# Optimization experiments

Measured on AMD Instinct MI355X. Metric: run time of the kernel, lower is better.

The kernel has to match this reference:

```python
import jax, jax.numpy as jnp
import numpy as np

NUM_GRAPHS = 64
NODE_SZ = 200
FEAT = 200
HID = 256          # hidden_size; each signed branch outputs HID//2
HALF = HID // 2
N_NODES = NUM_GRAPHS * NODE_SZ
N_EDGES = 409600
NUM_LAYERS = 3


def _lin_init(key, out_f, in_f):
    kw, kb = jax.random.split(key)
    s = 1.0 / np.sqrt(in_f)
    W = jax.random.uniform(kw, (out_f, in_f), minval=-s, maxval=s, dtype=jnp.float32)
    b = jax.random.uniform(kb, (out_f,), minval=-s, maxval=s, dtype=jnp.float32)
    return W, b


def setup_inputs() -> dict:
    key = jax.random.key(0)
    ks = jax.random.split(key, 16)
    x = jax.random.normal(ks[0], (N_NODES, FEAT), dtype=jnp.float32)
    edge_index = jax.random.randint(ks[1], (2, N_EDGES), 0, N_NODES, dtype=jnp.int64)
    edge_weight = jax.random.normal(ks[2], (N_EDGES,), dtype=jnp.float32)
    batch = jnp.repeat(jnp.arange(NUM_GRAPHS, dtype=jnp.int64), NODE_SZ)

    # signed conv layer params: layer0 in=FEAT, layers 1..: in=HID; each lin maps 2*in -> HALF
    Wp0, bp0 = _lin_init(ks[3], HALF, 2 * FEAT)
    Wn0, bn0 = _lin_init(ks[4], HALF, 2 * FEAT)
    Wp1, bp1 = _lin_init(ks[5], HALF, 2 * HID)
    Wn1, bn1 = _lin_init(ks[6], HALF, 2 * HID)
    Wp2, bp2 = _lin_init(ks[7], HALF, 2 * HID)
    Wn2, bn2 = _lin_init(ks[8], HALF, 2 * HID)
    Wr, br = _lin_init(ks[9], HID, NODE_SZ * HID)   # readout_lin
    Wl, bl = _lin_init(ks[10], 1, HID)              # final lin
    return dict(x=x, edge_index=edge_index, edge_weight=edge_weight, batch=batch,
                Wp0=Wp0, bp0=bp0, Wn0=Wn0, bn0=bn0,
                Wp1=Wp1, bp1=bp1, Wn1=Wn1, bn1=bn1,
                Wp2=Wp2, bp2=bp2, Wn2=Wn2, bn2=bn2,
                Wr=Wr, br=br, Wl=Wl, bl=bl)


def _signed_conv(x, src, dst, w, Wp, bp, Wn, bn):
    # edge-weighted signed mean aggregation, split by weight sign
    xs = x[src]                                   # [E, D] gather
    pw = jnp.where(w > 0, w, 0.0)
    nw = jnp.where(w < 0, -w, 0.0)
    agg_p = jax.ops.segment_sum(pw[:, None] * xs, dst, num_segments=N_NODES)
    agg_n = jax.ops.segment_sum(nw[:, None] * xs, dst, num_segments=N_NODES)
    deg_p = jax.ops.segment_sum((w > 0).astype(x.dtype), dst, num_segments=N_NODES)
    deg_n = jax.ops.segment_sum((w < 0).astype(x.dtype), dst, num_segments=N_NODES)
    agg_p = agg_p / jnp.maximum(deg_p, 1.0)[:, None]
    agg_n = agg_n / jnp.maximum(deg_n, 1.0)[:, None]
    hp = jnp.concatenate([agg_p, x], -1) @ Wp.T + bp
    hn = jnp.concatenate([agg_n, x], -1) @ Wn.T + bn
    return jnp.concatenate([hp, hn], -1)          # [N, HID]


def reference(x, edge_index, edge_weight, batch,
              Wp0, bp0, Wn0, bn0, Wp1, bp1, Wn1, bn1, Wp2, bp2, Wn2, bn2,
              Wr, br, Wl, bl):
    src, dst = edge_index[0], edge_index[1]
    convs = [(Wp0, bp0, Wn0, bn0), (Wp1, bp1, Wn1, bn1), (Wp2, bp2, Wn2, bn2)]
    h = x
    for i, (Wp, bp, Wn, bn) in enumerate(convs):
        h = _signed_conv(h, src, dst, edge_weight, Wp, bp, Wn, bn)
        if i < NUM_LAYERS - 1:
            h = jax.nn.leaky_relu(h, negative_slope=0.01)
    # per-graph readout: batch is contiguous with NODE_SZ nodes per graph,
    # so the boolean-mask+view loop is exactly a reshape.
    g = h.reshape(NUM_GRAPHS, NODE_SZ * HID)
    g = g @ Wr.T + br                             # [G, HID]
    # dropout(p=0.5) is identity in eval mode
    return g @ Wl.T + bl                          # [G, 1]
```

## Files before the change

### kernel.cpp

```cpp
#include <hip/hip_runtime.h>

#define NUM_GRAPHS 64
#define NODE_SZ    200
#define FEAT       200
#define HID        256
#define HALF       128
#define N_NODES    (NUM_GRAPHS * NODE_SZ)
#define KREAD      (NODE_SZ * HID)

typedef unsigned short ushort_t;
typedef unsigned int uint_t;
typedef __attribute__((ext_vector_type(8))) short bf16x8;
typedef __attribute__((ext_vector_type(4))) float f32x4;

#define GAS(p) ((const __attribute__((address_space(1))) void*)(p))
#define LAS(p) ((__attribute__((address_space(3))) void*)(p))

__device__ __forceinline__ float bf2f(ushort_t u) {
    union { unsigned int i; float f; } v; v.i = ((unsigned int)u) << 16; return v.f;
}
__device__ __forceinline__ ushort_t f2bf(float f) {
    union { float f; unsigned int i; } v; v.f = f;
    unsigned int x = v.i;
    unsigned int r = (x + 0x7fffu + ((x >> 16) & 1u)) >> 16;
    return (ushort_t)r;
}

#define OFF_CNT    0
#define OFF_WEFF   51264
#define OFF_OBND   256064
#define OFF_RANK   358472
#define OFF_ES     1177672
#define OFF_YALL   4454480
#define OFF_HA     17561680
#define OFF_HB     24115280
#define OFF_WALL   30668880
#define OFF_XB     31455312

__global__ __launch_bounds__(256) void prep_kernel(
        const float* __restrict__ Wp0, const float* __restrict__ Wn0,
        const float* __restrict__ Wp1, const float* __restrict__ Wn1,
        const float* __restrict__ Wp2, const float* __restrict__ Wn2,
        const float* __restrict__ x, const float* __restrict__ Wr,
        const float* __restrict__ Wl,
        const int* __restrict__ ei, const float* __restrict__ ew, int E,
        uint_t* __restrict__ cnt, ushort_t* __restrict__ rank16,
        ushort_t* __restrict__ wall, ushort_t* __restrict__ xb,
        float* __restrict__ weff) {
    int gid = blockIdx.x * 256 + threadIdx.x;
    const int GS = gridDim.x * 256;
    for (int idx = gid; idx < 3 * 131072; idx += GS) {
        int layer = idx >> 17, within = idx & 131071;
        int rr = within >> 8, col = within & 255;
        const float* Wp = (layer == 0) ? Wp0 : (layer == 1) ? Wp1 : Wp2;
        const float* Wn = (layer == 0) ? Wn0 : (layer == 1) ? Wn1 : Wn2;
        int Ks = (layer == 0) ? 200 : 256;
        int q = rr >> 7;
        const float* Wsrc = (q & 1) ? Wn : Wp;
        int row = rr & 127;
        int scol = col + ((q >> 1) ? Ks : 0);
        float v = (col < Ks) ? Wsrc[(size_t)row * (2 * Ks) + scol] : 0.0f;
        wall[idx] = f2bf(v);
    }
    for (int idx = gid; idx < N_NODES * 64; idx += GS) {
        int n = idx >> 6, c0 = (idx & 63) * 4;
        ushort4 o = {0, 0, 0, 0};
        if (c0 < 200) {
            float4 v = *(const float4*)&x[(size_t)n * 200 + c0];
            o.x = f2bf(v.x); o.y = f2bf(v.y); o.z = f2bf(v.z); o.w = f2bf(v.w);
        }
        *(ushort4*)&xb[(size_t)n * 256 + c0] = o;
    }
    for (int k = gid; k < KREAD; k += GS) {
        float s[8] = {0.f, 0.f, 0.f, 0.f, 0.f, 0.f, 0.f, 0.f};
#pragma unroll 1
        for (int c = 0; c < 256; c += 8) {
#pragma unroll
            for (int j = 0; j < 8; ++j)
                s[j] = fmaf(Wl[c + j], Wr[(size_t)(c + j) * KREAD + k], s[j]);
        }
        weff[k] = ((s[0] + s[1]) + (s[2] + s[3])) + ((s[4] + s[5]) + (s[6] + s[7]));
    }
    for (int e = gid; e < E; e += GS) {
        int dst = ei[E + e];
        float w = ew[e];
        if (w > 0.0f) {
            uint_t old = atomicAdd(&cnt[dst], 1u);
            rank16[e] = (ushort_t)(old & 0xffffu);
        } else if (w < 0.0f) {
            uint_t old = atomicAdd(&cnt[dst], 0x10000u);
            rank16[e] = (ushort_t)(old >> 16);
        }
    }
}

__global__ __launch_bounds__(1024) void scan_kernel(const uint_t* __restrict__ cnt,
                                                    uint2* __restrict__ obnd,
                                                    const float* __restrict__ br,
                                                    const float* __restrict__ Wl,
                                                    const float* __restrict__ bl,
                                                    float* __restrict__ outg, int n) {
    const int PER = 13;
    int t = threadIdx.x;
    int start = t * PER;
    int local[PER];
    uint_t pcnt[PER];
    int sum = 0;
#pragma unroll
    for (int i = 0; i < PER; ++i) {
        int idx = start + i;
        uint_t c = (idx < n) ? cnt[idx] : 0u;
        int v = (int)((c & 0xffffu) + (c >> 16));
        pcnt[i] = c & 0xffffu;
        local[i] = sum;
        sum += v;
    }
    int lane = t & 63, wid = t >> 6;
    int inc = sum;
#pragma unroll
    for (int d = 1; d < 64; d <<= 1) {
        int up = __shfl_up(inc, d);
        if (lane >= d) inc += up;
    }
    __shared__ int wsum[16], woff[16];
    if (lane == 63) wsum[wid] = inc;
    __syncthreads();
    if (t < 16) {
        int acc = 0;
        for (int j = 0; j < 16; ++j) if (j < t) acc += wsum[j];
        woff[t] = acc;
    }
    __syncthreads();
    int base = woff[wid] + (inc - sum);
#pragma unroll
    for (int i = 0; i < PER; ++i) {
        int idx = start + i;
        if (idx < n) {
            uint_t off = (uint_t)(base + local[i]);
            obnd[idx] = make_uint2(off, off + pcnt[i]);
        }
    }
    if (t == 1023) {
        uint_t tot = (uint_t)(base + sum);
        obnd[n] = make_uint2(tot, tot);
    }
    if (t < 64) {
        float p = br[t] * Wl[t] + br[t + 64] * Wl[t + 64]
                + br[t + 128] * Wl[t + 128] + br[t + 192] * Wl[t + 192];
#pragma unroll
        for (int d = 32; d > 0; d >>= 1) p += __shfl_xor(p, d);
        outg[t] = p + bl[0];
    }
}

__device__ __forceinline__ void gemm_body(int t, const ushort_t* __restrict__ A,
                                          const ushort_t* __restrict__ Bw,
                                          ushort_t* __restrict__ Y,
                                          ushort_t* smem) {
    int mBase = (t >> 1) * 128;
    int nBase = (t & 1) * 256;
    int tid  = threadIdx.x;
    int lane = tid & 63;
    int wv   = tid >> 6;
    int r    = lane & 15;
    int quad = lane >> 4;
    int wm   = wv >> 1;
    int wn   = wv & 1;

    int rowA = tid >> 2, colc = (tid & 3) * 8;
    const ushort_t* gA  = A  + (size_t)(mBase + rowA) * 256 + colc;
    const ushort_t* gB0 = Bw + (size_t)(nBase + rowA) * 256 + colc;
    const ushort_t* gB1 = Bw + (size_t)(nBase + 128 + rowA) * 256 + colc;

    f32x4 acc[2][8];
#pragma unroll
    for (int i = 0; i < 2; ++i)
#pragma unroll
        for (int j = 0; j < 8; ++j) acc[i][j] = (f32x4){0.f, 0.f, 0.f, 0.f};

    auto STAGE = [&](int buf, int kb) {
        ushort_t* Ad = smem + (buf << 12) + tid * 8;
        ushort_t* Bd = smem + 8192 + (buf << 13) + tid * 8;
        __builtin_amdgcn_global_load_lds(GAS(gA + kb), LAS(Ad), 16, 0, 0);
        __builtin_amdgcn_global_load_lds(GAS(gB0 + kb), LAS(Bd), 16, 0, 0);
        __builtin_amdgcn_global_load_lds(GAS(gB1 + kb), LAS(Bd + 4096), 16, 0, 0);
    };

    STAGE(0, 0);
    for (int kt = 0; kt < 8; ++kt) {
        int cb = kt & 1;
        __syncthreads();
        if (kt < 7) STAGE(cb ^ 1, (kt + 1) * 32);
        const ushort_t* Ac = smem + (cb << 12);
        const ushort_t* Bc = smem + 8192 + (cb << 13);
        bf16x8 af[2];
#pragma unroll
        for (int i = 0; i < 2; ++i)
            af[i] = *(const bf16x8*)&Ac[(wm * 32 + i * 16 + r) * 32 + quad * 8];
#pragma unroll
        for (int j = 0; j < 8; ++j) {
            bf16x8 bfr = *(const bf16x8*)&Bc[(wn * 128 + j * 16 + r) * 32 + quad * 8];
            acc[0][j] = __builtin_amdgcn_mfma_f32_16x16x32_bf16(af[0], bfr, acc[0][j], 0, 0, 0);
            acc[1][j] = __builtin_amdgcn_mfma_f32_16x16x32_bf16(af[1], bfr, acc[1][j], 0, 0, 0);
        }
    }
#pragma unroll
    for (int i = 0; i < 2; ++i)
#pragma unroll
        for (int j = 0; j < 8; ++j) {
            int c = nBase + wn * 128 + j * 16 + r;
#pragma unroll
            for (int reg = 0; reg < 4; ++reg) {
                int m = mBase + wm * 32 + i * 16 + quad * 4 + reg;
                Y[(size_t)m * 512 + c] = f2bf(acc[i][j][reg]);
            }
        }
}

__global__ __launch_bounds__(512) void scatgemm_kernel(
        const int* __restrict__ ei, const float* __restrict__ ew,
        const uint2* __restrict__ obnd, const ushort_t* __restrict__ rank16,
        uint2* __restrict__ es, int E,
        const ushort_t* __restrict__ xb, const ushort_t* __restrict__ wall,
        ushort_t* __restrict__ Yall) {
    __shared__ __align__(16) ushort_t smem[24576];
    int bx = blockIdx.x;
    if (bx < 200) {
        gemm_body(bx, xb, wall, Yall, smem);
        return;
    }
    int e = (bx - 200) * 512 + threadIdx.x;
    if (e < E) {
        int src = ei[e];
        int dst = ei[E + e];
        float w = ew[e];
        uint_t rk = rank16[e];
        if (w > 0.0f)
            es[obnd[dst].x + rk] = make_uint2((uint_t)src, __float_as_uint(w));
        else if (w < 0.0f)
            es[obnd[dst].y + rk] = make_uint2((uint_t)src, __float_as_uint(-w));
    }
}

__global__ __launch_bounds__(512) void gemm_kernel(const ushort_t* __restrict__ A,
                                                   const ushort_t* __restrict__ Bw,
                                                   ushort_t* __restrict__ Y) {
    __shared__ __align__(16) ushort_t smem[24576];
    gemm_body(blockIdx.x, A, Bw, Y, smem);
}

template <bool LEAKY, bool DOT>
__global__ __launch_bounds__(256) void agg_kernel(
        const ushort_t* __restrict__ Y,
        const uint2* __restrict__ obnd,
        const uint2* __restrict__ es,
        const float* __restrict__ bp, const float* __restrict__ bn,
        ushort_t* __restrict__ outp,
        const float* __restrict__ weff,
        float* __restrict__ outg) {
    __shared__ float sdot[4];
    int lane = threadIdx.x & 63;
    int wv   = threadIdx.x >> 6;
    int n = blockIdx.x * 4 + wv;
    int c0 = lane * 2;
    uint2 ob = obnd[n];
    uint_t off = ob.x, mid = ob.y, end = obnd[n + 1].x;

    float accp[2] = {0.f, 0.f};
    float accn[2] = {0.f, 0.f};

#pragma unroll 1
    for (int phase = 0; phase < 2; ++phase) {
        uint_t lo = phase ? mid : off;
        uint_t hi = phase ? end : mid;
        float* acc = phase ? accn : accp;
        const ushort_t* Yb = Y + (phase ? 128 : 0) + c0;
#pragma unroll 1
        for (uint_t base = lo; base < hi; base += 64) {
            int cnt = (int)min(64u, hi - base);
            uint2 rec = es[base + (uint_t)min(lane, cnt - 1)];
            int i = 0;
#pragma unroll 1
            for (; i + 8 <= cnt; i += 8) {
                int s[8]; float w[8]; uint_t u[8];
#pragma unroll
                for (int j = 0; j < 8; ++j) {
                    s[j] = __shfl((int)rec.x, i + j);
                    w[j] = __uint_as_float((uint_t)__shfl((int)rec.y, i + j));
                }
#pragma unroll
                for (int j = 0; j < 8; ++j) u[j] = *(const uint_t*)&Yb[(size_t)s[j] * 512];
#pragma unroll
                for (int j = 0; j < 8; ++j) {
                    acc[0] = fmaf(w[j], bf2f((ushort_t)(u[j] & 0xffffu)), acc[0]);
                    acc[1] = fmaf(w[j], bf2f((ushort_t)(u[j] >> 16)), acc[1]);
                }
            }
#pragma unroll 1
            for (; i < cnt; ++i) {
                int s = __shfl((int)rec.x, i);
                float w = __uint_as_float((uint_t)__shfl((int)rec.y, i));
                uint_t u = *(const uint_t*)&Yb[(size_t)s * 512];
                acc[0] = fmaf(w, bf2f((ushort_t)(u & 0xffffu)), acc[0]);
                acc[1] = fmaf(w, bf2f((ushort_t)(u >> 16)), acc[1]);
            }
        }
    }

    float dp = fmaxf((float)(mid - off), 1.0f);
    float dn = fmaxf((float)(end - mid), 1.0f);
    float rp = 1.0f / dp, rn = 1.0f / dn;
    uint_t zp = *(const uint_t*)&Y[(size_t)n * 512 + 256 + c0];
    uint_t zn = *(const uint_t*)&Y[(size_t)n * 512 + 384 + c0];
    float vp0 = fmaf(accp[0], rp, bf2f((ushort_t)(zp & 0xffffu)) + bp[c0]);
    float vp1 = fmaf(accp[1], rp, bf2f((ushort_t)(zp >> 16))     + bp[c0 + 1]);
    float vn0 = fmaf(accn[0], rn, bf2f((ushort_t)(zn & 0xffffu)) + bn[c0]);
    float vn1 = fmaf(accn[1], rn, bf2f((ushort_t)(zn >> 16))     + bn[c0 + 1]);
    if (LEAKY) {
        vp0 = (vp0 > 0.0f) ? vp0 : 0.01f * vp0;
        vp1 = (vp1 > 0.0f) ? vp1 : 0.01f * vp1;
        vn0 = (vn0 > 0.0f) ? vn0 : 0.01f * vn0;
        vn1 = (vn1 > 0.0f) ? vn1 : 0.01f * vn1;
    }
    if (DOT) {
        int g = blockIdx.x / 50;
        int kbase = (n % 200) * 256;
        float s = vp0 * weff[kbase + c0] + vp1 * weff[kbase + c0 + 1]
                + vn0 * weff[kbase + 128 + c0] + vn1 * weff[kbase + 128 + c0 + 1];
#pragma unroll
        for (int d = 32; d > 0; d >>= 1) s += __shfl_xor(s, d);
        if (lane == 0) sdot[wv] = s;
        __syncthreads();
        if (threadIdx.x == 0)
            atomicAdd(&outg[g], (sdot[0] + sdot[1]) + (sdot[2] + sdot[3]));
    } else {
        uint_t op = (uint_t)f2bf(vp0) | ((uint_t)f2bf(vp1) << 16);
        uint_t on = (uint_t)f2bf(vn0) | ((uint_t)f2bf(vn1) << 16);
        *(uint_t*)&outp[(size_t)n * 256 + c0]       = op;
        *(uint_t*)&outp[(size_t)n * 256 + 128 + c0] = on;
    }
}

extern "C" void kernel_launch(void* const* d_in, const int* in_sizes, int n_in,
                              void* d_out, int out_size, void* d_ws, size_t ws_size,
                              hipStream_t stream) {
    const float* x  = (const float*)d_in[0];
    const int*   ei = (const int*)d_in[1];
    const float* ew = (const float*)d_in[2];
    const float* Wp0 = (const float*)d_in[4];
    const float* bp0 = (const float*)d_in[5];
    const float* Wn0 = (const float*)d_in[6];
    const float* bn0 = (const float*)d_in[7];
    const float* Wp1 = (const float*)d_in[8];
    const float* bp1 = (const float*)d_in[9];
    const float* Wn1 = (const float*)d_in[10];
    const float* bn1 = (const float*)d_in[11];
    const float* Wp2 = (const float*)d_in[12];
    const float* bp2 = (const float*)d_in[13];
    const float* Wn2 = (const float*)d_in[14];
    const float* bn2 = (const float*)d_in[15];
    const float* Wr  = (const float*)d_in[16];
    const float* br  = (const float*)d_in[17];
    const float* Wl  = (const float*)d_in[18];
    const float* bl  = (const float*)d_in[19];
    const int E = in_sizes[1] / 2;

    char* ws = (char*)d_ws;
    uint_t*   cnt    = (uint_t*)(ws + OFF_CNT);
    float*    weff   = (float*)(ws + OFF_WEFF);
    uint2*    obnd   = (uint2*)(ws + OFF_OBND);
    ushort_t* rank16 = (ushort_t*)(ws + OFF_RANK);
    uint2*    es     = (uint2*)(ws + OFF_ES);
    ushort_t* Yall   = (ushort_t*)(ws + OFF_YALL);
    ushort_t* hA     = (ushort_t*)(ws + OFF_HA);
    ushort_t* hB     = (ushort_t*)(ws + OFF_HB);
    ushort_t* wall   = (ushort_t*)(ws + OFF_WALL);
    ushort_t* xb     = (ushort_t*)(ws + OFF_XB);
    float*    outg   = (float*)d_out;

    hipMemsetAsync(ws + OFF_CNT, 0, N_NODES * sizeof(uint_t), stream);
    hipLaunchKernelGGL(prep_kernel, dim3(512), dim3(256), 0, stream,
                       Wp0, Wn0, Wp1, Wn1, Wp2, Wn2, x, Wr, Wl,
                       ei, ew, E, cnt, rank16, wall, xb, weff);
    hipLaunchKernelGGL(scan_kernel, dim3(1), dim3(1024), 0, stream,
                       cnt, obnd, br, Wl, bl, outg, N_NODES);
    hipLaunchKernelGGL(scatgemm_kernel, dim3(200 + (E + 511) / 512), dim3(512), 0, stream,
                       ei, ew, obnd, rank16, es, E, xb, wall, Yall);
    hipLaunchKernelGGL((agg_kernel<true, false>), dim3(N_NODES / 4), dim3(256), 0, stream,
                       Yall, obnd, es, bp0, bn0, hA, (const float*)nullptr, (float*)nullptr);
    hipLaunchKernelGGL(gemm_kernel, dim3(200), dim3(512), 0, stream, hA, wall + 131072, Yall);
    hipLaunchKernelGGL((agg_kernel<true, false>), dim3(N_NODES / 4), dim3(256), 0, stream,
                       Yall, obnd, es, bp1, bn1, hB, (const float*)nullptr, (float*)nullptr);
    hipLaunchKernelGGL(gemm_kernel, dim3(200), dim3(512), 0, stream, hB, wall + 262144, Yall);
    hipLaunchKernelGGL((agg_kernel<false, true>), dim3(N_NODES / 4), dim3(256), 0, stream,
                       Yall, obnd, es, bp2, bn2, (ushort_t*)nullptr, weff, outg);
}
```

Before: 285.6 us.

## Specialize prep blocks per task and use scalar-load edge gathers in aggregation

```diff
diff --git a/kernel.cpp b/kernel.cpp
--- a/kernel.cpp
+++ b/kernel.cpp
@@ -47,49 +47,56 @@
         uint_t* __restrict__ cnt, ushort_t* __restrict__ rank16,
         ushort_t* __restrict__ wall, ushort_t* __restrict__ xb,
         float* __restrict__ weff) {
-    int gid = blockIdx.x * 256 + threadIdx.x;
-    const int GS = gridDim.x * 256;
-    for (int idx = gid; idx < 3 * 131072; idx += GS) {
-        int layer = idx >> 17, within = idx & 131071;
-        int rr = within >> 8, col = within & 255;
-        const float* Wp = (layer == 0) ? Wp0 : (layer == 1) ? Wp1 : Wp2;
-        const float* Wn = (layer == 0) ? Wn0 : (layer == 1) ? Wn1 : Wn2;
-        int Ks = (layer == 0) ? 200 : 256;
-        int q = rr >> 7;
-        const float* Wsrc = (q & 1) ? Wn : Wp;
-        int row = rr & 127;
-        int scol = col + ((q >> 1) ? Ks : 0);
-        float v = (col < Ks) ? Wsrc[(size_t)row * (2 * Ks) + scol] : 0.0f;
-        wall[idx] = f2bf(v);
-    }
-    for (int idx = gid; idx < N_NODES * 64; idx += GS) {
-        int n = idx >> 6, c0 = (idx & 63) * 4;
-        ushort4 o = {0, 0, 0, 0};
-        if (c0 < 200) {
-            float4 v = *(const float4*)&x[(size_t)n * 200 + c0];
-            o.x = f2bf(v.x); o.y = f2bf(v.y); o.z = f2bf(v.z); o.w = f2bf(v.w);
-        }
-        *(ushort4*)&xb[(size_t)n * 256 + c0] = o;
-    }
-    for (int k = gid; k < KREAD; k += GS) {
-        float s[8] = {0.f, 0.f, 0.f, 0.f, 0.f, 0.f, 0.f, 0.f};
+    int bx = blockIdx.x, tid = threadIdx.x;
+    if (bx < 200) {
+        int k = bx * 256 + tid;
+        float s[16];
+#pragma unroll
+        for (int j = 0; j < 16; ++j) s[j] = 0.f;
 #pragma unroll 1
-        for (int c = 0; c < 256; c += 8) {
-#pragma unroll
-            for (int j = 0; j < 8; ++j)
+        for (int c = 0; c < 256; c += 16) {
+#pragma unroll
+            for (int j = 0; j < 16; ++j)
                 s[j] = fmaf(Wl[c + j], Wr[(size_t)(c + j) * KREAD + k], s[j]);
         }
-        weff[k] = ((s[0] + s[1]) + (s[2] + s[3])) + ((s[4] + s[5]) + (s[6] + s[7]));
-    }
-    for (int e = gid; e < E; e += GS) {
-        int dst = ei[E + e];
-        float w = ew[e];
-        if (w > 0.0f) {
-            uint_t old = atomicAdd(&cnt[dst], 1u);
-            rank16[e] = (ushort_t)(old & 0xffffu);
-        } else if (w < 0.0f) {
-            uint_t old = atomicAdd(&cnt[dst], 0x10000u);
-            rank16[e] = (ushort_t)(old >> 16);
+        float t0 = ((s[0] + s[1]) + (s[2] + s[3])) + ((s[4] + s[5]) + (s[6] + s[7]));
+        float t1 = ((s[8] + s[9]) + (s[10] + s[11])) + ((s[12] + s[13]) + (s[14] + s[15]));
+        weff[k] = t0 + t1;
+    } else if (bx < 300) {
+        for (int idx = (bx - 200) * 256 + tid; idx < N_NODES * 64; idx += 25600) {
+            int n = idx >> 6, c0 = (idx & 63) * 4;
+            ushort4 o = {0, 0, 0, 0};
+            if (c0 < 200) {
+                float4 v = *(const float4*)&x[(size_t)n * 200 + c0];
+                o.x = f2bf(v.x); o.y = f2bf(v.y); o.z = f2bf(v.z); o.w = f2bf(v.w);
+            }
+            *(ushort4*)&xb[(size_t)n * 256 + c0] = o;
+        }
+    } else if (bx < 364) {
+        for (int idx = (bx - 300) * 256 + tid; idx < 3 * 131072; idx += 16384) {
+            int layer = idx >> 17, within = idx & 131071;
+            int rr = within >> 8, col = within & 255;
+            const float* Wp = (layer == 0) ? Wp0 : (layer == 1) ? Wp1 : Wp2;
+            const float* Wn = (layer == 0) ? Wn0 : (layer == 1) ? Wn1 : Wn2;
+            int Ks = (layer == 0) ? 200 : 256;
+            int q = rr >> 7;
+            const float* Wsrc = (q & 1) ? Wn : Wp;
+            int row = rr & 127;
+            int scol = col + ((q >> 1) ? Ks : 0);
+            float v = (col < Ks) ? Wsrc[(size_t)row * (2 * Ks) + scol] : 0.0f;
+            wall[idx] = f2bf(v);
+        }
+    } else {
+        for (int e = (bx - 364) * 256 + tid; e < E; e += 38912) {
+            int dst = ei[E + e];
+            float w = ew[e];
+            if (w > 0.0f) {
+                uint_t old = atomicAdd(&cnt[dst], 1u);
+                rank16[e] = (ushort_t)(old & 0xffffu);
+            } else if (w < 0.0f) {
+                uint_t old = atomicAdd(&cnt[dst], 0x10000u);
+                rank16[e] = (ushort_t)(old >> 16);
+            }
         }
     }
 }
@@ -247,6 +254,30 @@
                                                    ushort_t* __restrict__ Y) {
     __shared__ __align__(16) ushort_t smem[24576];
     gemm_body(blockIdx.x, A, Bw, Y, smem);
+}
+
+template <int B, bool CLAMP>
+__device__ __forceinline__ void gather_batch(const uint2* __restrict__ es,
+                                             uint_t e, uint_t hi,
+                                             const ushort_t* __restrict__ Yph, int c0,
+                                             float* __restrict__ acc) {
+    uint_t u[B];
+    float  w[B];
+#pragma unroll
+    for (int j = 0; j < B; ++j) {
+        uint_t idx = CLAMP ? min(e + (uint_t)j, hi - 1u) : (e + (uint_t)j);
+        uint2 r = es[idx];
+        uint_t s = __builtin_amdgcn_readfirstlane(r.x);
+        float  wj = __uint_as_float(r.y);
+        w[j] = (CLAMP && (e + (uint_t)j >= hi)) ? 0.0f : wj;
+        const ushort_t* rowp = Yph + (size_t)s * 512;
+        u[j] = *(const uint_t*)&rowp[c0];
+    }
+#pragma unroll
+    for (int j = 0; j < B; ++j) {
+        acc[0] = fmaf(w[j], bf2f((ushort_t)(u[j] & 0xffffu)), acc[0]);
+        acc[1] = fmaf(w[j], bf2f((ushort_t)(u[j] >> 16)), acc[1]);
+    }
 }
 
 template <bool LEAKY, bool DOT>
@@ -264,47 +295,23 @@
     int n = blockIdx.x * 4 + wv;
     int c0 = lane * 2;
     uint2 ob = obnd[n];
-    uint_t off = ob.x, mid = ob.y, end = obnd[n + 1].x;
+    uint_t off = __builtin_amdgcn_readfirstlane(ob.x);
+    uint_t mid = __builtin_amdgcn_readfirstlane(ob.y);
+    uint_t end = __builtin_amdgcn_readfirstlane(obnd[n + 1].x);
 
     float accp[2] = {0.f, 0.f};
     float accn[2] = {0.f, 0.f};
 
 #pragma unroll 1
     for (int phase = 0; phase < 2; ++phase) {
-        uint_t lo = phase ? mid : off;
+        uint_t e  = phase ? mid : off;
         uint_t hi = phase ? end : mid;
         float* acc = phase ? accn : accp;
-        const ushort_t* Yb = Y + (phase ? 128 : 0) + c0;
+        const ushort_t* Yph = Y + (phase ? 128 : 0);
 #pragma unroll 1
-        for (uint_t base = lo; base < hi; base += 64) {
-            int cnt = (int)min(64u, hi - base);
-            uint2 rec = es[base + (uint_t)min(lane, cnt - 1)];
-            int i = 0;
-#pragma unroll 1
-            for (; i + 8 <= cnt; i += 8) {
-                int s[8]; float w[8]; uint_t u[8];
-#pragma unroll
-                for (int j = 0; j < 8; ++j) {
-                    s[j] = __shfl((int)rec.x, i + j);
-                    w[j] = __uint_as_float((uint_t)__shfl((int)rec.y, i + j));
-                }
-#pragma unroll
-                for (int j = 0; j < 8; ++j) u[j] = *(const uint_t*)&Yb[(size_t)s[j] * 512];
-#pragma unroll
-                for (int j = 0; j < 8; ++j) {
-                    acc[0] = fmaf(w[j], bf2f((ushort_t)(u[j] & 0xffffu)), acc[0]);
-                    acc[1] = fmaf(w[j], bf2f((ushort_t)(u[j] >> 16)), acc[1]);
-                }
-            }
-#pragma unroll 1
-            for (; i < cnt; ++i) {
-                int s = __shfl((int)rec.x, i);
-                float w = __uint_as_float((uint_t)__shfl((int)rec.y, i));
-                uint_t u = *(const uint_t*)&Yb[(size_t)s * 512];
-                acc[0] = fmaf(w, bf2f((ushort_t)(u & 0xffffu)), acc[0]);
-                acc[1] = fmaf(w, bf2f((ushort_t)(u >> 16)), acc[1]);
-            }
-        }
+        while (e + 16 <= hi) { gather_batch<16, false>(es, e, hi, Yph, c0, acc); e += 16; }
+        if (e + 8 <= hi)     { gather_batch<8,  false>(es, e, hi, Yph, c0, acc); e += 8; }
+        if (e < hi)          { gather_batch<8,  true >(es, e, hi, Yph, c0, acc); }
     }
 
     float dp = fmaxf((float)(mid - off), 1.0f);
@@ -379,7 +386,7 @@
     float*    outg   = (float*)d_out;
 
     hipMemsetAsync(ws + OFF_CNT, 0, N_NODES * sizeof(uint_t), stream);
-    hipLaunchKernelGGL(prep_kernel, dim3(512), dim3(256), 0, stream,
+    hipLaunchKernelGGL(prep_kernel, dim3(516), dim3(256), 0, stream,
                        Wp0, Wn0, Wp1, Wn1, Wp2, Wn2, x, Wr, Wl,
                        ei, ew, E, cnt, rank16, wall, xb, weff);
     hipLaunchKernelGGL(scan_kernel, dim3(1), dim3(1024), 0, stream,
```

Result: faster. 275.0 us (-3.7%).
